# Kernel optimization log

Hardware: AMD Instinct MI355X
Metric: run time of the kernel (lower is better)

## Reference

```python
import jax, jax.numpy as jnp
import numpy as np

N, E = 50000, 800000
IN, C, H, EDIM = 128, 16, 8, 8  # in_channels, out_channels per head, heads, edge_dim
NEG_SLOPE = 0.2


def setup_inputs() -> dict:
    key = jax.random.key(0)
    ks = jax.random.split(key, 10)
    g = 1.0 / np.sqrt(IN)
    inp = {
        "x": jax.random.normal(ks[0], (N, IN), dtype=jnp.float32),
        "edge_index": jax.random.randint(ks[1], (2, E), 0, N, dtype=jnp.int64),
        "edge_attr": jax.random.normal(ks[2], (E, EDIM), dtype=jnp.float32),
        # GATv2Conv params (share_weights=False): lin_l, lin_r with bias, lin_edge no bias
        "W_l": jax.random.normal(ks[3], (IN, H * C), dtype=jnp.float32) * g,
        "b_l": jnp.zeros((H * C,), dtype=jnp.float32),
        "W_r": jax.random.normal(ks[4], (IN, H * C), dtype=jnp.float32) * g,
        "b_r": jnp.zeros((H * C,), dtype=jnp.float32),
        "W_e": jax.random.normal(ks[5], (EDIM, H * C), dtype=jnp.float32) * (1.0 / np.sqrt(EDIM)),
        "att": jax.random.normal(ks[6], (H, C), dtype=jnp.float32) * (1.0 / np.sqrt(C)),
        "bias": jnp.zeros((H * C,), dtype=jnp.float32),
    }
    return inp


def _gatv2_forward(x, edge_index, edge_attr, W_l, b_l, W_r, b_r, W_e, att, bias):
    n = x.shape[0]
    x_l = (x @ W_l + b_l).reshape(n, H, C)  # source transform
    x_r = (x @ W_r + b_r).reshape(n, H, C)  # target transform

    # add self-loops; edge_attr fill_value='mean' (PyG GATv2Conv default)
    loop = jnp.arange(n, dtype=edge_index.dtype)
    src = jnp.concatenate([edge_index[0], loop])
    dst = jnp.concatenate([edge_index[1], loop])
    loop_attr = jnp.broadcast_to(edge_attr.mean(axis=0, keepdims=True), (n, EDIM))
    e_attr = jnp.concatenate([edge_attr, loop_attr], axis=0)  # [E+N, EDIM]

    e_emb = (e_attr @ W_e).reshape(-1, H, C)  # [E+N, H, C]
    m = x_l[src] + x_r[dst] + e_emb          # gather per edge
    m = jax.nn.leaky_relu(m, NEG_SLOPE)
    logit = jnp.einsum("ehc,hc->eh", m, att)  # [E+N, H]

    # destination-grouped (scatter) softmax
    seg_max = jax.ops.segment_max(logit, dst, num_segments=n)
    expd = jnp.exp(logit - seg_max[dst])
    seg_sum = jax.ops.segment_sum(expd, dst, num_segments=n)
    alpha = expd / (seg_sum[dst] + 1e-16)     # [E+N, H]

    msg = alpha[:, :, None] * x_l[src]        # [E+N, H, C]
    out = jax.ops.segment_sum(msg, dst, num_segments=n)  # [N, H, C]
    return out.reshape(n, H * C) + bias       # concat heads + bias


def reference(x, edge_index, edge_attr, W_l, b_l, W_r, b_r, W_e, att, bias):
    return _gatv2_forward(x, edge_index, edge_attr, W_l, b_l, W_r, b_r, W_e, att, bias)
```

## Files before the change

kernel.cpp:

```cpp
#include <hip/hip_runtime.h>

#define NHEAD 8
#define CH    16
#define HC    128
#define INC   128
#define EDIM  8
#define NEG   0.2f

typedef _Float16 h8 __attribute__((ext_vector_type(8)));
typedef _Float16 h2 __attribute__((ext_vector_type(2)));
typedef float    f4 __attribute__((ext_vector_type(4)));

__device__ __forceinline__ float dot2(h2 a, h2 b, float c) {
#if __has_builtin(__builtin_amdgcn_fdot2)
    return __builtin_amdgcn_fdot2(a, b, c, false);
#else
    return c + (float)a[0] * (float)b[0] + (float)a[1] * (float)b[1];
#endif
}

__global__ __launch_bounds__(256) void k_histpack(
        const float* __restrict__ Wl, const float* __restrict__ Wr,
        const float* __restrict__ We, const float* __restrict__ att,
        _Float16* __restrict__ packed, _Float16* __restrict__ We16, _Float16* __restrict__ att16,
        const int* __restrict__ ei, const float* __restrict__ ea,
        int* __restrict__ cnt, int* __restrict__ rank, float* __restrict__ attr_sum,
        int E) {
    __shared__ float red[4][8];
    if ((int)blockIdx.x < 16) {
        int id = blockIdx.x * 256 + threadIdx.x;
        int l  = id & 63;
        int kb = (id >> 6) & 3;
        int t  = id >> 8;
        int col = t * 16 + (l & 15);
        const float* W = (col < HC) ? Wl : Wr;
        int c = col & 127;
        int kbase = kb * 32 + (l >> 4) * 8;
        _Float16* dst = packed + (size_t)id * 8;
        #pragma unroll
        for (int j = 0; j < 8; ++j) dst[j] = (_Float16)W[(size_t)(kbase + j) * HC + c];
        if (id < 1024) We16[id] = (_Float16)We[id];
        if (id < 128)  att16[id] = (_Float16)att[id];
    } else {
        int t = (blockIdx.x - 16) * 256 + threadIdx.x;
        float av[8] = {0.f, 0.f, 0.f, 0.f, 0.f, 0.f, 0.f, 0.f};
        if (t < E) {
            rank[t] = atomicAdd(&cnt[ei[E + t]], 1);
            float4 a0 = *(const float4*)(ea + (size_t)t * EDIM);
            float4 a1 = *(const float4*)(ea + (size_t)t * EDIM + 4);
            av[0] = a0.x; av[1] = a0.y; av[2] = a0.z; av[3] = a0.w;
            av[4] = a1.x; av[5] = a1.y; av[6] = a1.z; av[7] = a1.w;
        }
        #pragma unroll
        for (int m = 1; m < 64; m <<= 1) {
            #pragma unroll
            for (int k = 0; k < 8; ++k) av[k] += __shfl_xor(av[k], m);
        }
        int lane = threadIdx.x & 63, wid = threadIdx.x >> 6;
        if (lane == 0) {
            #pragma unroll
            for (int k = 0; k < 8; ++k) red[wid][k] = av[k];
        }
        __syncthreads();
        if (threadIdx.x < 8) {
            float s = red[0][threadIdx.x] + red[1][threadIdx.x] + red[2][threadIdx.x] + red[3][threadIdx.x];
            atomicAdd(&attr_sum[threadIdx.x], s);
        }
    }
}

__global__ void k_scan1(const int* __restrict__ cnt, int* __restrict__ off,
                        int* __restrict__ bsum, int N,
                        const float* __restrict__ attr_sum, const float* __restrict__ We,
                        _Float16* __restrict__ loop16, float invE) {
    __shared__ int wpre[16];
    int i = blockIdx.x * 1024 + threadIdx.x;
    int lane = threadIdx.x & 63, wid = threadIdx.x >> 6;
    int v = (i < N) ? cnt[i] : 0;
    int s = v;
    #pragma unroll
    for (int d = 1; d < 64; d <<= 1) {
        int t = __shfl_up(s, d);
        if (lane >= d) s += t;
    }
    if (lane == 63) wpre[wid] = s;
    __syncthreads();
    if (threadIdx.x == 0) {
        int run = 0;
        #pragma unroll
        for (int q = 0; q < 16; ++q) { int t = wpre[q]; wpre[q] = run; run += t; }
        bsum[blockIdx.x] = run;
    }
    __syncthreads();
    if (i <= N) off[i] = wpre[wid] + s - v;

    if (blockIdx.x == 0 && threadIdx.x < HC) {
        int j = threadIdx.x;
        float acc = 0.f;
        #pragma unroll
        for (int d = 0; d < EDIM; ++d) acc += attr_sum[d] * invE * We[d * HC + j];
        loop16[j] = (_Float16)acc;
    }
}

__global__ __launch_bounds__(256) void k_phase2(
        const float* __restrict__ x, const _Float16* __restrict__ packed,
        const float* __restrict__ bl, const float* __restrict__ br,
        _Float16* __restrict__ xh,
        const int* __restrict__ ei, const float* __restrict__ ea,
        const int* __restrict__ off, const int* __restrict__ bsum,
        const int* __restrict__ rank,
        int* __restrict__ esrc, h8* __restrict__ eac,
        int N, int E, int gemmBlocks, int nb) {
    __shared__ _Float16 st[16][264];

    if ((int)blockIdx.x < gemmBlocks) {
        int nb0 = blockIdx.x * 64;
        int w  = threadIdx.x >> 6;
        int l  = threadIdx.x & 63;

        const h8* pk = (const h8*)packed;
        h8 bfrag[4][4];
        #pragma unroll
        for (int t4 = 0; t4 < 4; ++t4)
            #pragma unroll
            for (int kb = 0; kb < 4; ++kb)
                bfrag[t4][kb] = pk[(size_t)(((w * 4 + t4) * 4 + kb) * 64 + l)];

        float bv[4];
        int cl = l & 15;
        #pragma unroll
        for (int t4 = 0; t4 < 4; ++t4) {
            int col = w * 64 + t4 * 16 + cl;
            bv[t4] = (col < HC) ? bl[col] : br[col - HC];
        }

        int g = l >> 4;
        int r0 = g * 4;
        for (int mt = 0; mt < 4; ++mt) {
            int m0 = nb0 + mt * 16;
            if (m0 >= N) break;
            int row = m0 + cl; if (row >= N) row = N - 1;
            const float* xp = x + (size_t)row * INC + g * 8;
            h8 afrag[4];
            #pragma unroll
            for (int kb = 0; kb < 4; ++kb) {
                float4 u = *(const float4*)(xp + kb * 32);
                float4 v = *(const float4*)(xp + kb * 32 + 4);
                h8 a;
                a[0] = (_Float16)u.x; a[1] = (_Float16)u.y; a[2] = (_Float16)u.z; a[3] = (_Float16)u.w;
                a[4] = (_Float16)v.x; a[5] = (_Float16)v.y; a[6] = (_Float16)v.z; a[7] = (_Float16)v.w;
                afrag[kb] = a;
            }
            f4 acc[4];
            #pragma unroll
            for (int t4 = 0; t4 < 4; ++t4) { f4 z = {0.f, 0.f, 0.f, 0.f}; acc[t4] = z; }
            #pragma unroll
            for (int kb = 0; kb < 4; ++kb)
                #pragma unroll
                for (int t4 = 0; t4 < 4; ++t4)
                    acc[t4] = __builtin_amdgcn_mfma_f32_16x16x32_f16(afrag[kb], bfrag[t4][kb], acc[t4], 0, 0, 0);
            #pragma unroll
            for (int t4 = 0; t4 < 4; ++t4) {
                int col = w * 64 + t4 * 16 + cl;
                #pragma unroll
                for (int j = 0; j < 4; ++j)
                    st[r0 + j][col] = (_Float16)(acc[t4][j] + bv[t4]);
            }
            __syncthreads();
            #pragma unroll
            for (int q = 0; q < 2; ++q) {
                int cch = threadIdx.x + 256 * q;
                int r = cch >> 5, ch = (cch & 31) * 8;
                int node = m0 + r;
                if (node < N) *(h8*)(xh + (size_t)node * 256 + ch) = *(const h8*)&st[r][ch];
            }
            __syncthreads();
        }
    } else {
        int lane = threadIdx.x & 63;
        int bv = (lane < nb) ? bsum[lane] : 0;
        int s = bv;
        #pragma unroll
        for (int d = 1; d < 64; d <<= 1) {
            int t = __shfl_up(s, d);
            if (lane >= d) s += t;
        }
        s -= bv;

        int t = (blockIdx.x - gemmBlocks) * 256 + threadIdx.x;
        if (t >= E) return;
        int dst = ei[E + t];
        int pos = off[dst] + __shfl(s, dst >> 10) + rank[t];
        esrc[pos] = ei[t];
        float4 a0 = *(const float4*)(ea + (size_t)t * EDIM);
        float4 a1 = *(const float4*)(ea + (size_t)t * EDIM + 4);
        h8 v;
        v[0] = (_Float16)a0.x; v[1] = (_Float16)a0.y; v[2] = (_Float16)a0.z; v[3] = (_Float16)a0.w;
        v[4] = (_Float16)a1.x; v[5] = (_Float16)a1.y; v[6] = (_Float16)a1.z; v[7] = (_Float16)a1.w;
        eac[pos] = v;
    }
}

__global__ __launch_bounds__(256) void k_gather(
        const int* __restrict__ esrc, const h8* __restrict__ eac,
        const _Float16* __restrict__ We16, const _Float16* __restrict__ att16,
        const _Float16* __restrict__ xh, const _Float16* __restrict__ loop16,
        const float* __restrict__ bias,
        const int* __restrict__ off, const int* __restrict__ bsum,
        float* __restrict__ out, int N, int nb) {
    int wid = (blockIdx.x * blockDim.x + threadIdx.x) >> 6;
    int lane = threadIdx.x & 63;
    int dstA = wid * 2;
    if (dstA >= N) return;
    dstA = __builtin_amdgcn_readfirstlane(dstA);
    bool hasB = (dstA + 1) < N;
    int dstB = hasB ? dstA + 1 : dstA;

    int qid = lane >> 4;
    int l   = lane & 15;
    int c0  = l * 8;

    int bv = (lane < nb) ? bsum[lane] : 0;
    int sx = bv;
    #pragma unroll
    for (int d = 1; d < 64; d <<= 1) {
        int t = __shfl_up(sx, d);
        if (lane >= d) sx += t;
    }
    sx -= bv;

    h8 we8[EDIM];
    #pragma unroll
    for (int d = 0; d < EDIM; ++d) we8[d] = *(const h8*)(We16 + d * HC + c0);
    h8 av8 = *(const h8*)(att16 + c0);
    h2 att2[4];
    #pragma unroll
    for (int k = 0; k < 4; ++k) { att2[k][0] = av8[2 * k]; att2[k][1] = av8[2 * k + 1]; }
    h8 lp8 = *(const h8*)(loop16 + c0);
    const h8 z8 = {};
    h8 ng8;
    #pragma unroll
    for (int k = 0; k < 8; ++k) ng8[k] = (_Float16)NEG;

    h8 xrA = *(const h8*)(xh + (size_t)dstA * 256 + HC + c0);
    h8 xrB = *(const h8*)(xh + (size_t)dstB * 256 + HC + c0);

    float accA[8] = {0.f, 0.f, 0.f, 0.f, 0.f, 0.f, 0.f, 0.f};
    float accB[8] = {0.f, 0.f, 0.f, 0.f, 0.f, 0.f, 0.f, 0.f};
    float segA = 0.f, segB = 0.f;

    auto TAIL = [&](h8 m8, h8 x8, bool valid, float (&av)[8], float &sw) {
        h8 mp = __builtin_elementwise_max(m8, z8);
        h8 mn = __builtin_elementwise_min(m8, z8);
        m8 = mp + mn * ng8;
        float p = 0.f;
        #pragma unroll
        for (int k = 0; k < 4; ++k) {
            h2 mm; mm[0] = m8[2 * k]; mm[1] = m8[2 * k + 1];
            p = dot2(mm, att2[k], p);
        }
        p += __shfl_xor(p, 1);
        float w = valid ? __expf(p) : 0.f;
        sw += w;
        #pragma unroll
        for (int k = 0; k < 8; ++k) av[k] += w * (float)x8[k];
    };

    {
        h8 x8 = *(const h8*)(xh + (size_t)dstA * 256 + c0);
        TAIL(x8 + xrA + lp8, x8, qid == 0, accA, segA);
    }
    {
        h8 x8 = *(const h8*)(xh + (size_t)dstB * 256 + c0);
        TAIL(x8 + xrB + lp8, x8, hasB && qid == 0, accB, segB);
    }

    int begA = off[dstA] + __shfl(sx, dstA >> 10);
    int endA = off[dstA + 1] + __shfl(sx, (dstA + 1) >> 10);
    int begB = begA, endB = begA;
    if (hasB) {
        begB = endA;
        endB = off[dstA + 2] + __shfl(sx, (dstA + 2) >> 10);
    }

    if (begA < endA || begB < endB) {
        int lastA = endA - 1, lastB = endB - 1;
        bool okA = endA > begA, okB = endB > begB;
        auto IDXA = [&](int i) { int j = i + qid; j = (j > lastA) ? lastA : j; return okA ? j : 0; };
        auto IDXB = [&](int i) { int j = i + qid; j = (j > lastB) ? lastB : j; return okB ? j : 0; };

        int jA = IDXA(begA), jB = IDXB(begB);
        int sA = esrc[jA]; h8 aA = eac[jA];
        int sB = esrc[jB]; h8 aB = eac[jB];
        h8 xA = *(const h8*)(xh + (size_t)sA * 256 + c0);
        h8 xB = *(const h8*)(xh + (size_t)sB * 256 + c0);

        int iA = begA, iB = begB;
        while (iA < endA || iB < endB) {
            int jnA = IDXA(iA + 4), jnB = IDXB(iB + 4);
            int snA = esrc[jnA]; h8 anA = eac[jnA];
            int snB = esrc[jnB]; h8 anB = eac[jnB];
            h8 xnA = *(const h8*)(xh + (size_t)snA * 256 + c0);
            h8 xnB = *(const h8*)(xh + (size_t)snB * 256 + c0);

            {
                h8 m8 = xA + xrA;
                #pragma unroll
                for (int d = 0; d < EDIM; ++d) {
                    h8 ad = {aA[d], aA[d], aA[d], aA[d], aA[d], aA[d], aA[d], aA[d]};
                    m8 += ad * we8[d];
                }
                TAIL(m8, xA, (iA + qid) < endA, accA, segA);
            }
            {
                h8 m8 = xB + xrB;
                #pragma unroll
                for (int d = 0; d < EDIM; ++d) {
                    h8 ad = {aB[d], aB[d], aB[d], aB[d], aB[d], aB[d], aB[d], aB[d]};
                    m8 += ad * we8[d];
                }
                TAIL(m8, xB, (iB + qid) < endB, accB, segB);
            }
            aA = anA; xA = xnA; aB = anB; xB = xnB;
            iA += 4; iB += 4;
        }
    }

    segA += __shfl_xor(segA, 16); segA += __shfl_xor(segA, 32);
    segB += __shfl_xor(segB, 16); segB += __shfl_xor(segB, 32);
    #pragma unroll
    for (int k = 0; k < 8; ++k) {
        accA[k] += __shfl_xor(accA[k], 16); accA[k] += __shfl_xor(accA[k], 32);
        accB[k] += __shfl_xor(accB[k], 16); accB[k] += __shfl_xor(accB[k], 32);
    }

    if (qid == 0) {
        f4 b0 = *(const f4*)(bias + c0), b1 = *(const f4*)(bias + c0 + 4);
        {
            float inv = 1.f / (segA + 1e-16f);
            f4 o0, o1;
            o0[0] = accA[0] * inv + b0[0]; o0[1] = accA[1] * inv + b0[1];
            o0[2] = accA[2] * inv + b0[2]; o0[3] = accA[3] * inv + b0[3];
            o1[0] = accA[4] * inv + b1[0]; o1[1] = accA[5] * inv + b1[1];
            o1[2] = accA[6] * inv + b1[2]; o1[3] = accA[7] * inv + b1[3];
            *(f4*)(out + (size_t)dstA * HC + c0)     = o0;
            *(f4*)(out + (size_t)dstA * HC + c0 + 4) = o1;
        }
        if (hasB) {
            float inv = 1.f / (segB + 1e-16f);
            f4 o0, o1;
            o0[0] = accB[0] * inv + b0[0]; o0[1] = accB[1] * inv + b0[1];
            o0[2] = accB[2] * inv + b0[2]; o0[3] = accB[3] * inv + b0[3];
            o1[0] = accB[4] * inv + b1[0]; o1[1] = accB[5] * inv + b1[1];
            o1[2] = accB[6] * inv + b1[2]; o1[3] = accB[7] * inv + b1[3];
            *(f4*)(out + (size_t)dstB * HC + c0)     = o0;
            *(f4*)(out + (size_t)dstB * HC + c0 + 4) = o1;
        }
    }
}

extern "C" void kernel_launch(void* const* d_in, const int* in_sizes, int n_in,
                              void* d_out, int out_size, void* d_ws, size_t ws_size,
                              hipStream_t stream) {
    int N = in_sizes[0] / INC;
    int E = in_sizes[1] / 2;
    const float* x    = (const float*)d_in[0];
    const int*   ei   = (const int*)d_in[1];
    const float* ea   = (const float*)d_in[2];
    const float* Wl   = (const float*)d_in[3];
    const float* bl   = (const float*)d_in[4];
    const float* Wr   = (const float*)d_in[5];
    const float* br   = (const float*)d_in[6];
    const float* We   = (const float*)d_in[7];
    const float* att  = (const float*)d_in[8];
    const float* bias = (const float*)d_in[9];
    float* out = (float*)d_out;

    _Float16* xh      = (_Float16*)d_ws;
    h8*       eac     = (h8*)(xh + (size_t)N * 256);
    float* attr_sum   = (float*)(eac + E);
    int*   cnt        = (int*)(attr_sum + 8);
    _Float16* loop16  = (_Float16*)(cnt + N);
    _Float16* packed  = loop16 + 128;
    _Float16* We16    = packed + 32768;
    _Float16* att16   = We16 + 1024;
    int*   off        = (int*)(att16 + 128);
    int*   rank       = off + (N + 2);
    int*   esrc       = rank + E;
    int*   bsum       = esrc + E;

    hipMemsetAsync(attr_sum, 0, (8 + (size_t)N) * sizeof(float), stream);

    int histBlocks = (E + 255) / 256;
    k_histpack<<<16 + histBlocks, 256, 0, stream>>>(Wl, Wr, We, att, packed, We16, att16,
                                                    ei, ea, cnt, rank, attr_sum, E);

    int nb = (N + 1 + 1023) / 1024;
    k_scan1<<<nb, 1024, 0, stream>>>(cnt, off, bsum, N, attr_sum, We, loop16, 1.0f / (float)E);

    int gemmBlocks = (N + 63) / 64;
    k_phase2<<<gemmBlocks + histBlocks, 256, 0, stream>>>(x, packed, bl, br, xh,
                                                          ei, ea, off, bsum, rank,
                                                          esrc, eac, N, E, gemmBlocks, nb);

    int waves = (N + 1) / 2;
    k_gather<<<((size_t)waves * 64 + 255) / 256, 256, 0, stream>>>(esrc, eac, We16, att16, xh, loop16,
                                                                   bias, off, bsum, out, N, nb);
}
```

Measured before the change: 163.2 us.

## Move edge-attr mean reduction into scatter pass and compute loop embedding in gather

The edge_attr column-sum reduction moves from the histogram kernel into the edge scatter branch of phase2, which already loads edge_attr, so each edge row is read once instead of twice. The self-loop embedding is no longer precomputed in the scan kernel; each gather wave rebuilds it from attr_sum and the fp16 We rows it already holds, which adds a little per-wave arithmetic and changes the rounding to fp16. The GEMM blocks in phase2 now process 128 rows instead of 64, halving the number of GEMM blocks and the per-block reloads of the packed weight fragments.

```diff
diff --git a/kernel.cpp b/kernel.cpp
--- a/kernel.cpp
+++ b/kernel.cpp
@@ -23,10 +23,8 @@
         const float* __restrict__ Wl, const float* __restrict__ Wr,
         const float* __restrict__ We, const float* __restrict__ att,
         _Float16* __restrict__ packed, _Float16* __restrict__ We16, _Float16* __restrict__ att16,
-        const int* __restrict__ ei, const float* __restrict__ ea,
-        int* __restrict__ cnt, int* __restrict__ rank, float* __restrict__ attr_sum,
-        int E) {
-    __shared__ float red[4][8];
+        const int* __restrict__ ei,
+        int* __restrict__ cnt, int* __restrict__ rank, int E) {
     if ((int)blockIdx.x < 16) {
         int id = blockIdx.x * 256 + threadIdx.x;
         int l  = id & 63;
@@ -43,36 +41,12 @@
         if (id < 128)  att16[id] = (_Float16)att[id];
     } else {
         int t = (blockIdx.x - 16) * 256 + threadIdx.x;
-        float av[8] = {0.f, 0.f, 0.f, 0.f, 0.f, 0.f, 0.f, 0.f};
-        if (t < E) {
-            rank[t] = atomicAdd(&cnt[ei[E + t]], 1);
-            float4 a0 = *(const float4*)(ea + (size_t)t * EDIM);
-            float4 a1 = *(const float4*)(ea + (size_t)t * EDIM + 4);
-            av[0] = a0.x; av[1] = a0.y; av[2] = a0.z; av[3] = a0.w;
-            av[4] = a1.x; av[5] = a1.y; av[6] = a1.z; av[7] = a1.w;
-        }
-        #pragma unroll
-        for (int m = 1; m < 64; m <<= 1) {
-            #pragma unroll
-            for (int k = 0; k < 8; ++k) av[k] += __shfl_xor(av[k], m);
-        }
-        int lane = threadIdx.x & 63, wid = threadIdx.x >> 6;
-        if (lane == 0) {
-            #pragma unroll
-            for (int k = 0; k < 8; ++k) red[wid][k] = av[k];
-        }
-        __syncthreads();
-        if (threadIdx.x < 8) {
-            float s = red[0][threadIdx.x] + red[1][threadIdx.x] + red[2][threadIdx.x] + red[3][threadIdx.x];
-            atomicAdd(&attr_sum[threadIdx.x], s);
-        }
+        if (t < E) rank[t] = atomicAdd(&cnt[ei[E + t]], 1);
     }
 }
 
 __global__ void k_scan1(const int* __restrict__ cnt, int* __restrict__ off,
-                        int* __restrict__ bsum, int N,
-                        const float* __restrict__ attr_sum, const float* __restrict__ We,
-                        _Float16* __restrict__ loop16, float invE) {
+                        int* __restrict__ bsum, int N) {
     __shared__ int wpre[16];
     int i = blockIdx.x * 1024 + threadIdx.x;
     int lane = threadIdx.x & 63, wid = threadIdx.x >> 6;
@@ -93,14 +67,6 @@
     }
     __syncthreads();
     if (i <= N) off[i] = wpre[wid] + s - v;
-
-    if (blockIdx.x == 0 && threadIdx.x < HC) {
-        int j = threadIdx.x;
-        float acc = 0.f;
-        #pragma unroll
-        for (int d = 0; d < EDIM; ++d) acc += attr_sum[d] * invE * We[d * HC + j];
-        loop16[j] = (_Float16)acc;
-    }
 }
 
 __global__ __launch_bounds__(256) void k_phase2(
@@ -110,12 +76,13 @@
         const int* __restrict__ ei, const float* __restrict__ ea,
         const int* __restrict__ off, const int* __restrict__ bsum,
         const int* __restrict__ rank,
-        int* __restrict__ esrc, h8* __restrict__ eac,
+        int* __restrict__ esrc, h8* __restrict__ eac, float* __restrict__ attr_sum,
         int N, int E, int gemmBlocks, int nb) {
     __shared__ _Float16 st[16][264];
+    __shared__ float red[4][8];
 
     if ((int)blockIdx.x < gemmBlocks) {
-        int nb0 = blockIdx.x * 64;
+        int nb0 = blockIdx.x * 128;
         int w  = threadIdx.x >> 6;
         int l  = threadIdx.x & 63;
 
@@ -137,7 +104,7 @@
 
         int g = l >> 4;
         int r0 = g * 4;
-        for (int mt = 0; mt < 4; ++mt) {
+        for (int mt = 0; mt < 8; ++mt) {
             int m0 = nb0 + mt * 16;
             if (m0 >= N) break;
             int row = m0 + cl; if (row >= N) row = N - 1;
@@ -189,26 +156,45 @@
         s -= bv;
 
         int t = (blockIdx.x - gemmBlocks) * 256 + threadIdx.x;
-        if (t >= E) return;
-        int dst = ei[E + t];
-        int pos = off[dst] + __shfl(s, dst >> 10) + rank[t];
-        esrc[pos] = ei[t];
-        float4 a0 = *(const float4*)(ea + (size_t)t * EDIM);
-        float4 a1 = *(const float4*)(ea + (size_t)t * EDIM + 4);
-        h8 v;
-        v[0] = (_Float16)a0.x; v[1] = (_Float16)a0.y; v[2] = (_Float16)a0.z; v[3] = (_Float16)a0.w;
-        v[4] = (_Float16)a1.x; v[5] = (_Float16)a1.y; v[6] = (_Float16)a1.z; v[7] = (_Float16)a1.w;
-        eac[pos] = v;
+        float av[8] = {0.f, 0.f, 0.f, 0.f, 0.f, 0.f, 0.f, 0.f};
+        if (t < E) {
+            int dst = ei[E + t];
+            int pos = off[dst] + __shfl(s, dst >> 10) + rank[t];
+            esrc[pos] = ei[t];
+            float4 a0 = *(const float4*)(ea + (size_t)t * EDIM);
+            float4 a1 = *(const float4*)(ea + (size_t)t * EDIM + 4);
+            av[0] = a0.x; av[1] = a0.y; av[2] = a0.z; av[3] = a0.w;
+            av[4] = a1.x; av[5] = a1.y; av[6] = a1.z; av[7] = a1.w;
+            h8 v;
+            #pragma unroll
+            for (int k = 0; k < 8; ++k) v[k] = (_Float16)av[k];
+            eac[pos] = v;
+        }
+        #pragma unroll
+        for (int m = 1; m < 64; m <<= 1) {
+            #pragma unroll
+            for (int k = 0; k < 8; ++k) av[k] += __shfl_xor(av[k], m);
+        }
+        int wv = threadIdx.x >> 6;
+        if (lane == 0) {
+            #pragma unroll
+            for (int k = 0; k < 8; ++k) red[wv][k] = av[k];
+        }
+        __syncthreads();
+        if (threadIdx.x < 8) {
+            float sm = red[0][threadIdx.x] + red[1][threadIdx.x] + red[2][threadIdx.x] + red[3][threadIdx.x];
+            atomicAdd(&attr_sum[threadIdx.x], sm);
+        }
     }
 }
 
 __global__ __launch_bounds__(256) void k_gather(
         const int* __restrict__ esrc, const h8* __restrict__ eac,
         const _Float16* __restrict__ We16, const _Float16* __restrict__ att16,
-        const _Float16* __restrict__ xh, const _Float16* __restrict__ loop16,
+        const _Float16* __restrict__ xh, const float* __restrict__ attr_sum,
         const float* __restrict__ bias,
         const int* __restrict__ off, const int* __restrict__ bsum,
-        float* __restrict__ out, int N, int nb) {
+        float* __restrict__ out, int N, int nb, float invE) {
     int wid = (blockIdx.x * blockDim.x + threadIdx.x) >> 6;
     int lane = threadIdx.x & 63;
     int dstA = wid * 2;
@@ -237,7 +223,13 @@
     h2 att2[4];
     #pragma unroll
     for (int k = 0; k < 4; ++k) { att2[k][0] = av8[2 * k]; att2[k][1] = av8[2 * k + 1]; }
-    h8 lp8 = *(const h8*)(loop16 + c0);
+    h8 lp8 = {};
+    #pragma unroll
+    for (int d = 0; d < EDIM; ++d) {
+        _Float16 md = (_Float16)(attr_sum[d] * invE);
+        h8 ms = {md, md, md, md, md, md, md, md};
+        lp8 += ms * we8[d];
+    }
     const h8 z8 = {};
     h8 ng8;
     #pragma unroll
@@ -381,8 +373,7 @@
     h8*       eac     = (h8*)(xh + (size_t)N * 256);
     float* attr_sum   = (float*)(eac + E);
     int*   cnt        = (int*)(attr_sum + 8);
-    _Float16* loop16  = (_Float16*)(cnt + N);
-    _Float16* packed  = loop16 + 128;
+    _Float16* packed  = (_Float16*)(cnt + N);
     _Float16* We16    = packed + 32768;
     _Float16* att16   = We16 + 1024;
     int*   off        = (int*)(att16 + 128);
@@ -394,17 +385,19 @@
 
     int histBlocks = (E + 255) / 256;
     k_histpack<<<16 + histBlocks, 256, 0, stream>>>(Wl, Wr, We, att, packed, We16, att16,
-                                                    ei, ea, cnt, rank, attr_sum, E);
+                                                    ei, cnt, rank, E);
 
     int nb = (N + 1 + 1023) / 1024;
-    k_scan1<<<nb, 1024, 0, stream>>>(cnt, off, bsum, N, attr_sum, We, loop16, 1.0f / (float)E);
-
-    int gemmBlocks = (N + 63) / 64;
+    k_scan1<<<nb, 1024, 0, stream>>>(cnt, off, bsum, N);
+
+    int gemmBlocks = (N + 127) / 128;
     k_phase2<<<gemmBlocks + histBlocks, 256, 0, stream>>>(x, packed, bl, br, xh,
                                                           ei, ea, off, bsum, rank,
-                                                          esrc, eac, N, E, gemmBlocks, nb);
+                                                          esrc, eac, attr_sum,
+                                                          N, E, gemmBlocks, nb);
 
     int waves = (N + 1) / 2;
-    k_gather<<<((size_t)waves * 64 + 255) / 256, 256, 0, stream>>>(esrc, eac, We16, att16, xh, loop16,
-                                                                   bias, off, bsum, out, N, nb);
-}
+    k_gather<<<((size_t)waves * 64 + 255) / 256, 256, 0, stream>>>(esrc, eac, We16, att16, xh,
+                                                                   attr_sum, bias, off, bsum,
+                                                                   out, N, nb, 1.0f / (float)E);
+}
```

After: 163.1 us. Within noise of the previous version (-0.1%).
